# Performance work log

Measured on AMD Instinct MI355X. Metric: run time of the kernel, lower is better.

The kernel has to match this reference:

```python
import jax, jax.numpy as jnp
import numpy as np

NL = 8      # num layers (['self','cross']*4)
H = 8       # heads
EPS = 1e-5  # torch LayerNorm default


def _layernorm(x, g, b):
    mu = jnp.mean(x, axis=-1, keepdims=True)
    var = jnp.mean((x - mu) ** 2, axis=-1, keepdims=True)
    return (x - mu) * jax.lax.rsqrt(var + EPS) * g + b


def _encoder_layer(x, source, Wq, Wk, Wv, Wm, W1, W2, g1, b1, g2, b2):
    # x: [N, L, C], source: [N, S, C]
    N, L, C = x.shape
    D = C // H
    q = (x @ Wq).reshape(N, L, H, D)
    k = (source @ Wk).reshape(N, -1, H, D)
    v = (source @ Wv).reshape(N, -1, H, D)
    # naive full attention: explicit [N, L, S, H] scores (as in FullAttention)
    qk = jnp.einsum('nlhd,nshd->nlsh', q, k)
    A = jax.nn.softmax(qk * (1.0 / np.sqrt(D)), axis=2)
    msg = jnp.einsum('nlsh,nshd->nlhd', A, v).reshape(N, L, C)
    msg = _layernorm(msg @ Wm, g1, b1)
    m = jnp.concatenate([x, msg], axis=-1)          # [N, L, 2C]
    m = jax.nn.relu(m @ W1) @ W2                    # [N, L, C]
    m = _layernorm(m, g2, b2)
    return x + m


def _loftr(feat0, feat1, Wq, Wk, Wv, Wm, W1, W2, g1, b1, g2, b2):
    names = ['self', 'cross'] * 4
    for i, name in enumerate(names):
        p = (Wq[i], Wk[i], Wv[i], Wm[i], W1[i], W2[i], g1[i], b1[i], g2[i], b2[i])
        if name == 'self':
            feat0 = _encoder_layer(feat0, feat0, *p)
            feat1 = _encoder_layer(feat1, feat1, *p)
        else:  # cross; note feat0 is updated before being fed to feat1's layer
            feat0 = _encoder_layer(feat0, feat1, *p)
            feat1 = _encoder_layer(feat1, feat0, *p)
    return jnp.stack([feat0, feat1], axis=0)  # [2, N, L, C]


def setup_inputs() -> dict:
    key = jax.random.key(0)
    ks = jax.random.split(key, 10)
    N, L, C = 8, 1024, 768
    s = 1.0 / np.sqrt(C)       # xavier-ish scale for [C, C]
    s2 = 1.0 / np.sqrt(2 * C)  # for MLP fan-in 2C
    return {
        'feat0': jax.random.normal(ks[0], (N, L, C), jnp.float32),
        'feat1': jax.random.normal(ks[1], (N, L, C), jnp.float32),
        'Wq': jax.random.normal(ks[2], (NL, C, C), jnp.float32) * s,
        'Wk': jax.random.normal(ks[3], (NL, C, C), jnp.float32) * s,
        'Wv': jax.random.normal(ks[4], (NL, C, C), jnp.float32) * s,
        'Wm': jax.random.normal(ks[5], (NL, C, C), jnp.float32) * s,
        'W1': jax.random.normal(ks[6], (NL, 2 * C, 2 * C), jnp.float32) * s2,
        'W2': jax.random.normal(ks[7], (NL, 2 * C, C), jnp.float32) * s2,
        'g1': jnp.ones((NL, C), jnp.float32),
        'b1': jnp.zeros((NL, C), jnp.float32),
        'g2': jnp.ones((NL, C), jnp.float32),
        'b2': jnp.zeros((NL, C), jnp.float32),
    }


def reference(feat0, feat1, Wq, Wk, Wv, Wm, W1, W2, g1, b1, g2, b2):
    return _loftr(feat0, feat1, Wq, Wk, Wv, Wm, W1, W2, g1, b1, g2, b2)
```

## Files before the change

### kernel.cpp

```cpp
#include <hip/hip_runtime.h>
#include <hip/hip_bf16.h>

typedef __hip_bfloat16 bf16;
typedef __bf16 bf16x8 __attribute__((ext_vector_type(8)));
typedef float f32x4 __attribute__((ext_vector_type(4)));

#define AS1 __attribute__((address_space(1)))
#define AS3 __attribute__((address_space(3)))
__device__ __forceinline__ void gl_lds16(const void* g, void* l) {
    __builtin_amdgcn_global_load_lds((const AS1 void*)g, (AS3 void*)l, 16, 0, 0);
}

__device__ __forceinline__ float fexp2(float x) {
#if __has_builtin(__builtin_amdgcn_exp2f)
    return __builtin_amdgcn_exp2f(x);
#else
    return exp2f(x);
#endif
}

__device__ __forceinline__ float bf16_lo(unsigned w) { return __uint_as_float(w << 16); }
__device__ __forceinline__ float bf16_hi(unsigned w) { return __uint_as_float(w & 0xffff0000u); }

__device__ __forceinline__ int xcd_swz(int did, int nwg) {
    return (did & 7) * (nwg >> 3) + (did >> 3);
}


__global__ __launch_bounds__(256) void cvt_f32_bf16_k(const float* __restrict__ in, bf16* __restrict__ out,
                                                      int ostride, int total, float* __restrict__ xout)
{
    int i = blockIdx.x * 256 + threadIdx.x;
    int e = i * 4;
    if (e >= total) return;
    int row = e / 768;
    int col = e - row * 768;
    const float4 f = *(const float4*)(in + e);
    bf16 o4[4];
    o4[0] = __float2bfloat16(f.x); o4[1] = __float2bfloat16(f.y);
    o4[2] = __float2bfloat16(f.z); o4[3] = __float2bfloat16(f.w);
    *(uint2*)(out + (size_t)row * ostride + col) = *(uint2*)o4;
    if (xout) *(float4*)(xout + e) = f;
}

__global__ void transpose_cvt_k(const float* __restrict__ in, bf16* __restrict__ out, int R, int C,
                                float scale, size_t lstride)
{
    __shared__ float t[32][33];
    const int tx = threadIdx.x, ty = threadIdx.y;
    in  += (size_t)blockIdx.z * R * C;
    out += (size_t)blockIdx.z * lstride;
    const int c0 = blockIdx.x * 32, r0 = blockIdx.y * 32;
    #pragma unroll
    for (int i = 0; i < 4; ++i)
        t[ty + i*8][tx] = in[(size_t)(r0 + ty + i*8) * C + c0 + tx];
    __syncthreads();
    #pragma unroll
    for (int i = 0; i < 4; ++i)
        out[(size_t)(c0 + ty + i*8) * R + r0 + tx] = __float2bfloat16(t[tx][ty + i*8] * scale);
}

template<int EPI>
__global__ __launch_bounds__(256) void gemm_bt_k(const bf16* __restrict__ A, int lda,
                                                 const bf16* __restrict__ BT, int K,
                                                 void* __restrict__ Cp, int ldc,
                                                 bf16* __restrict__ Ck, bf16* __restrict__ Cv,
                                                 const bf16* __restrict__ A2)
{
    __shared__ bf16 a_sm[3][4096];
    __shared__ bf16 b_sm[3][4096];
    const int tid = threadIdx.x;
    const int lane = tid & 63;
    const int wid = tid >> 6;
    const int wr = wid >> 1, wc = wid & 1;

    const int nwg = gridDim.x * gridDim.y;
    const int did = blockIdx.x + gridDim.x * blockIdx.y;
    const int wgid = xcd_swz(did, nwg);
    const int col0 = (wgid % gridDim.y) * 128;
    const int row0 = (wgid / gridDim.y) * 128;
    const int g = lane >> 4, r16 = lane & 15;

    if (EPI == 4 && col0 >= 768) A = A2;

    const int r4 = lane >> 2;
    const int sc = (lane & 3) ^ ((lane >> 3) & 3);
    const bf16* gA[2]; const bf16* gB[2]; int loff[2];
    #pragma unroll
    for (int i = 0; i < 2; ++i) {
        const int blk = wid*2 + i;
        gA[i] = A  + (size_t)(row0 + blk*16 + r4) * lda + sc*8;
        gB[i] = BT + (size_t)(col0 + blk*16 + r4) * K   + sc*8;
        loff[i] = blk * 512;
    }
    const int foff = r16*32 + ((g ^ ((r16 >> 1) & 3)) * 8);

    f32x4 acc[4][4];
    #pragma unroll
    for (int m = 0; m < 4; ++m)
        #pragma unroll
        for (int n = 0; n < 4; ++n)
            #pragma unroll
            for (int r = 0; r < 4; ++r) acc[m][n][r] = 0.f;

    #pragma unroll
    for (int i = 0; i < 2; ++i) {
        gl_lds16(gA[i],      &a_sm[0][loff[i]]);
        gl_lds16(gB[i],      &b_sm[0][loff[i]]);
    }
    #pragma unroll
    for (int i = 0; i < 2; ++i) {
        gl_lds16(gA[i] + 32, &a_sm[1][loff[i]]);
        gl_lds16(gB[i] + 32, &b_sm[1][loff[i]]);
    }

    int cur = 0, pre = 2;
    for (int k0 = 0; k0 < K; k0 += 32) {
        if (k0 + 32 < K) asm volatile("s_waitcnt vmcnt(4)" ::: "memory");
        else             asm volatile("s_waitcnt vmcnt(0)" ::: "memory");
        __builtin_amdgcn_s_barrier();
        if (k0 + 64 < K) {
            #pragma unroll
            for (int i = 0; i < 2; ++i) {
                gl_lds16(gA[i] + k0 + 64, &a_sm[pre][loff[i]]);
                gl_lds16(gB[i] + k0 + 64, &b_sm[pre][loff[i]]);
            }
        }
        bf16x8 af[4], bfr[4];
        #pragma unroll
        for (int m = 0; m < 4; ++m) af[m]  = *(const bf16x8*)&a_sm[cur][(wr*4 + m)*512 + foff];
        #pragma unroll
        for (int n = 0; n < 4; ++n) bfr[n] = *(const bf16x8*)&b_sm[cur][(wc*4 + n)*512 + foff];
        asm volatile("s_waitcnt lgkmcnt(0)" ::: "memory");
        __builtin_amdgcn_s_setprio(1);
        #pragma unroll
        for (int m = 0; m < 4; ++m)
            #pragma unroll
            for (int n = 0; n < 4; ++n)
                acc[m][n] = __builtin_amdgcn_mfma_f32_16x16x32_bf16(af[m], bfr[n], acc[m][n], 0, 0, 0);
        __builtin_amdgcn_s_setprio(0);
        cur = (cur == 2) ? 0 : cur + 1;
        pre = (pre == 2) ? 0 : pre + 1;
    }

    #pragma unroll
    for (int m = 0; m < 4; ++m) {
        const int orow = row0 + wr*64 + m*16 + g*4;
        #pragma unroll
        for (int n = 0; n < 4; ++n) {
            const int ocol = col0 + wc*64 + n*16 + r16;
            if (EPI == 4) {
                const int seg = ocol / 768;
                const int ci = ocol - seg*768;
                if (seg <= 1) {
                    bf16* dst = (seg == 0) ? (bf16*)Cp : Ck;
                    #pragma unroll
                    for (int r = 0; r < 4; ++r)
                        dst[(size_t)(orow + r)*768 + ci] = __float2bfloat16(acc[m][n][r]);
                } else {
                    const int nn = orow >> 10, ss = orow & 1023;
                    const int hh = ci / 96, dd = ci - hh * 96;
                    bf16 pk[4];
                    #pragma unroll
                    for (int r = 0; r < 4; ++r) pk[r] = __float2bfloat16(acc[m][n][r]);
                    *(uint2*)&Cv[(((size_t)nn*8 + hh)*96 + dd)*1024 + ss] = *(uint2*)pk;
                }
            } else {
                #pragma unroll
                for (int r = 0; r < 4; ++r) {
                    float v = acc[m][n][r];
                    if (EPI == 1) v = fmaxf(v, 0.f);
                    ((bf16*)Cp)[(size_t)(orow + r)*ldc + ocol] = __float2bfloat16(v);
                }
            }
        }
    }
}

__global__ __launch_bounds__(512) void attn_k(const bf16* __restrict__ qb, const bf16* __restrict__ kb,
                                              const bf16* __restrict__ vtb, bf16* __restrict__ msgb)
{
    __shared__ bf16 kv_sm[3][12*512];
    __shared__ bf16 p_sm_all[8][32][40];
    const int tid = threadIdx.x;
    const int lane = tid & 63;
    const int w = tid >> 6;
    const int g = lane >> 4, r16 = lane & 15;

    const int nwg = gridDim.x * gridDim.y;
    const int did = blockIdx.x + gridDim.x * blockIdx.y;
    const int wgid = xcd_swz(did, nwg);
    const int qx = wgid % gridDim.x;
    const int nh = wgid / gridDim.x;
    const int n = nh >> 3, h = nh & 7;
    const int q0 = qx * 256 + w * 32;

    bf16 (*p_sm)[40] = p_sm_all[w];

    const bf16* kbase = kb  + ((size_t)n*1024)*768 + (size_t)h*96;
    const bf16* vbase = vtb + ((size_t)(n*8 + h))*96*1024;

    bf16x8 aq[2][3];
    #pragma unroll
    for (int qh = 0; qh < 2; ++qh) {
        const size_t qoff = ((size_t)n*1024 + q0 + qh*16 + r16) * 768 + (size_t)h*96;
        #pragma unroll
        for (int c = 0; c < 3; ++c) aq[qh][c] = *(const bf16x8*)&qb[qoff + c*32 + g*8];
    }

    const int r4 = lane >> 2;
    const int sc = (lane & 3) ^ ((lane >> 3) & 3);
    const bf16* gsrc[2]; size_t gstep[2]; int dstoff[2];
    const int nissue = (w < 4) ? 2 : 1;
    #pragma unroll
    for (int jj = 0; jj < 2; ++jj) {
        const int issue = w + jj*8;
        if (issue < 6) {
            const int c = issue >> 1, kh = issue & 1;
            gsrc[jj]  = kbase + (size_t)(kh*16 + r4)*768 + c*32 + sc*8;
            gstep[jj] = 768;
        } else {
            gsrc[jj]  = vbase + (size_t)((issue-6)*16 + r4)*1024 + sc*8;
            gstep[jj] = 1;
        }
        dstoff[jj] = (issue < 12) ? issue * 512 : 0;
    }
    const int foff = r16*32 + ((g ^ ((r16 >> 1) & 3)) * 8);

    float m_run[2], l_run[2];
    #pragma unroll
    for (int qh = 0; qh < 2; ++qh) { m_run[qh] = -1e30f; l_run[qh] = 0.f; }
    f32x4 o[2][6];
    #pragma unroll
    for (int qg = 0; qg < 2; ++qg)
        #pragma unroll
        for (int f = 0; f < 6; ++f)
            #pragma unroll
            for (int r = 0; r < 4; ++r) o[qg][f][r] = 0.f;

    gl_lds16(gsrc[0], &kv_sm[0][dstoff[0]]);
    if (nissue == 2) gl_lds16(gsrc[1], &kv_sm[0][dstoff[1]]);
    gl_lds16(gsrc[0] + 32 * gstep[0], &kv_sm[1][dstoff[0]]);
    if (nissue == 2) gl_lds16(gsrc[1] + 32 * gstep[1], &kv_sm[1][dstoff[1]]);

    int cur = 0, pre = 2;
    for (int kt = 0; kt < 1024; kt += 32) {
        if (kt + 32 < 1024) {
            if (nissue == 2) asm volatile("s_waitcnt vmcnt(2)" ::: "memory");
            else             asm volatile("s_waitcnt vmcnt(1)" ::: "memory");
        } else {
            asm volatile("s_waitcnt vmcnt(0)" ::: "memory");
        }
        __builtin_amdgcn_s_barrier();
        if (kt + 64 < 1024) {
            gl_lds16(gsrc[0] + (size_t)(kt + 64) * gstep[0], &kv_sm[pre][dstoff[0]]);
            if (nissue == 2) gl_lds16(gsrc[1] + (size_t)(kt + 64) * gstep[1], &kv_sm[pre][dstoff[1]]);
        }
        const bf16* rd = kv_sm[cur];

        f32x4 s[2][2];
        #pragma unroll
        for (int kh = 0; kh < 2; ++kh)
            #pragma unroll
            for (int qh = 0; qh < 2; ++qh)
                #pragma unroll
                for (int r = 0; r < 4; ++r) s[kh][qh][r] = 0.f;
        __builtin_amdgcn_s_setprio(1);
        #pragma unroll
        for (int c = 0; c < 3; ++c) {
            bf16x8 ak0 = *(const bf16x8*)&rd[(c*2 + 0)*512 + foff];
            bf16x8 ak1 = *(const bf16x8*)&rd[(c*2 + 1)*512 + foff];
            s[0][0] = __builtin_amdgcn_mfma_f32_16x16x32_bf16(ak0, aq[0][c], s[0][0], 0, 0, 0);
            s[0][1] = __builtin_amdgcn_mfma_f32_16x16x32_bf16(ak0, aq[1][c], s[0][1], 0, 0, 0);
            s[1][0] = __builtin_amdgcn_mfma_f32_16x16x32_bf16(ak1, aq[0][c], s[1][0], 0, 0, 0);
            s[1][1] = __builtin_amdgcn_mfma_f32_16x16x32_bf16(ak1, aq[1][c], s[1][1], 0, 0, 0);
        }
        __builtin_amdgcn_s_setprio(0);

        float pmv[2], gr[2];
        #pragma unroll
        for (int qh = 0; qh < 2; ++qh) {
            float pm = fmaxf(fmaxf(fmaxf(s[0][qh][0], s[0][qh][1]), fmaxf(s[0][qh][2], s[0][qh][3])),
                             fmaxf(fmaxf(s[1][qh][0], s[1][qh][1]), fmaxf(s[1][qh][2], s[1][qh][3])));
            pm = fmaxf(pm, __shfl_xor(pm, 16, 64));
            pm = fmaxf(pm, __shfl_xor(pm, 32, 64));
            pmv[qh] = pm;
            gr[qh] = pm - m_run[qh];
        }
        if (__any(fmaxf(gr[0], gr[1]) > 8.0f)) {
            float alpha_c[2];
            #pragma unroll
            for (int qh = 0; qh < 2; ++qh) {
                float mn = fmaxf(m_run[qh], pmv[qh]);
                alpha_c[qh] = fexp2(m_run[qh] - mn);
                m_run[qh] = mn;
                l_run[qh] *= alpha_c[qh];
            }
            #pragma unroll
            for (int qg = 0; qg < 2; ++qg)
                #pragma unroll
                for (int r = 0; r < 4; ++r) {
                    float ar = __shfl(alpha_c[qg], g*4 + r, 64);
                    #pragma unroll
                    for (int f = 0; f < 6; ++f) o[qg][f][r] *= ar;
                }
        }
        #pragma unroll
        for (int qh = 0; qh < 2; ++qh) {
            bf16 pk0[4], pk1[4];
            float rs = 0.f;
            #pragma unroll
            for (int r = 0; r < 4; ++r) {
                float p0 = fexp2(s[0][qh][r] - m_run[qh]);
                float p1 = fexp2(s[1][qh][r] - m_run[qh]);
                rs += p0 + p1;
                pk0[r] = __float2bfloat16(p0);
                pk1[r] = __float2bfloat16(p1);
            }
            rs += __shfl_xor(rs, 16, 64);
            rs += __shfl_xor(rs, 32, 64);
            l_run[qh] += rs;
            *(uint2*)&p_sm[qh*16 + r16][g*4]      = *(uint2*)pk0;
            *(uint2*)&p_sm[qh*16 + r16][16 + g*4] = *(uint2*)pk1;
        }

        bf16x8 pa0 = *(const bf16x8*)&p_sm[r16][g*8];
        bf16x8 pa1 = *(const bf16x8*)&p_sm[16 + r16][g*8];
        __builtin_amdgcn_s_setprio(1);
        #pragma unroll
        for (int f = 0; f < 6; ++f) {
            bf16x8 bv = *(const bf16x8*)&rd[(6 + f)*512 + foff];
            o[0][f] = __builtin_amdgcn_mfma_f32_16x16x32_bf16(pa0, bv, o[0][f], 0, 0, 0);
            o[1][f] = __builtin_amdgcn_mfma_f32_16x16x32_bf16(pa1, bv, o[1][f], 0, 0, 0);
        }
        __builtin_amdgcn_s_setprio(0);
        asm volatile("s_waitcnt lgkmcnt(0)" ::: "memory");
        cur = (cur == 2) ? 0 : cur + 1;
        pre = (pre == 2) ? 0 : pre + 1;
    }

    float linv[2][4];
    #pragma unroll
    for (int qg = 0; qg < 2; ++qg)
        #pragma unroll
        for (int r = 0; r < 4; ++r)
            linv[qg][r] = 1.0f / __shfl(l_run[qg], g*4 + r, 64);

    #pragma unroll
    for (int qg = 0; qg < 2; ++qg) {
        const size_t obase = ((size_t)n*1024 + q0 + qg*16 + g*4) * 768 + (size_t)h*96;
        #pragma unroll
        for (int f = 0; f < 6; ++f)
            #pragma unroll
            for (int r = 0; r < 4; ++r)
                msgb[obase + (size_t)r*768 + f*16 + r16] = __float2bfloat16(o[qg][f][r] * linv[qg][r]);
    }
}

template<int MODE>
__global__ __launch_bounds__(256) void ln_k(const bf16* __restrict__ in, const float* __restrict__ g,
                                            const float* __restrict__ b, bf16* __restrict__ outc,
                                            float* __restrict__ x)
{
    const int lane = threadIdx.x & 63;
    const int w = threadIdx.x >> 6;
    const int row = blockIdx.x * 4 + w;
    const bf16* rp = in + (size_t)row * 768;
    const int c1 = lane * 8, c2 = 512 + lane * 4;

    const uint4 u1 = *(const uint4*)&rp[c1];
    const uint2 u2 = *(const uint2*)&rp[c2];
    float f1[8], f2[4];
    f1[0] = bf16_lo(u1.x); f1[1] = bf16_hi(u1.x);
    f1[2] = bf16_lo(u1.y); f1[3] = bf16_hi(u1.y);
    f1[4] = bf16_lo(u1.z); f1[5] = bf16_hi(u1.z);
    f1[6] = bf16_lo(u1.w); f1[7] = bf16_hi(u1.w);
    f2[0] = bf16_lo(u2.x); f2[1] = bf16_hi(u2.x);
    f2[2] = bf16_lo(u2.y); f2[3] = bf16_hi(u2.y);
    float s = 0.f, sq = 0.f;
    #pragma unroll
    for (int j = 0; j < 8; ++j) { s += f1[j]; sq += f1[j]*f1[j]; }
    #pragma unroll
    for (int j = 0; j < 4; ++j) { s += f2[j]; sq += f2[j]*f2[j]; }
    #pragma unroll
    for (int off = 1; off < 64; off <<= 1) {
        s  += __shfl_xor(s,  off, 64);
        sq += __shfl_xor(sq, off, 64);
    }
    const float mu = s * (1.f/768.f);
    float var = sq * (1.f/768.f) - mu*mu;
    var = fmaxf(var, 0.f);
    const float rs = rsqrtf(var + 1e-5f);

    const float4 ga  = *(const float4*)&g[c1];
    const float4 gb4 = *(const float4*)&g[c1 + 4];
    const float4 gc  = *(const float4*)&g[c2];
    const float4 ba  = *(const float4*)&b[c1];
    const float4 bb4 = *(const float4*)&b[c1 + 4];
    const float4 bc  = *(const float4*)&b[c2];
    float y1[8], y2[4];
    y1[0] = (f1[0]-mu)*rs*ga.x + ba.x;   y1[1] = (f1[1]-mu)*rs*ga.y + ba.y;
    y1[2] = (f1[2]-mu)*rs*ga.z + ba.z;   y1[3] = (f1[3]-mu)*rs*ga.w + ba.w;
    y1[4] = (f1[4]-mu)*rs*gb4.x + bb4.x; y1[5] = (f1[5]-mu)*rs*gb4.y + bb4.y;
    y1[6] = (f1[6]-mu)*rs*gb4.z + bb4.z; y1[7] = (f1[7]-mu)*rs*gb4.w + bb4.w;
    y2[0] = (f2[0]-mu)*rs*gc.x + bc.x;   y2[1] = (f2[1]-mu)*rs*gc.y + bc.y;
    y2[2] = (f2[2]-mu)*rs*gc.z + bc.z;   y2[3] = (f2[3]-mu)*rs*gc.w + bc.w;

    if (MODE == 1) {
        bf16 o1[8], o2[4];
        #pragma unroll
        for (int j = 0; j < 8; ++j) o1[j] = __float2bfloat16(y1[j]);
        #pragma unroll
        for (int j = 0; j < 4; ++j) o2[j] = __float2bfloat16(y2[j]);
        *(uint4*)&outc[(size_t)row*1536 + 768 + c1] = *(uint4*)o1;
        *(uint2*)&outc[(size_t)row*1536 + 768 + c2] = *(uint2*)o2;
    } else {
        float* xr = x + (size_t)row * 768;
        float4 xa = *(float4*)&xr[c1];
        float4 xb = *(float4*)&xr[c1 + 4];
        float4 xc = *(float4*)&xr[c2];
        xa.x += y1[0]; xa.y += y1[1]; xa.z += y1[2]; xa.w += y1[3];
        xb.x += y1[4]; xb.y += y1[5]; xb.z += y1[6]; xb.w += y1[7];
        xc.x += y2[0]; xc.y += y2[1]; xc.z += y2[2]; xc.w += y2[3];
        *(float4*)&xr[c1]     = xa;
        *(float4*)&xr[c1 + 4] = xb;
        *(float4*)&xr[c2]     = xc;
        bf16 o1[8], o2[4];
        o1[0] = __float2bfloat16(xa.x); o1[1] = __float2bfloat16(xa.y);
        o1[2] = __float2bfloat16(xa.z); o1[3] = __float2bfloat16(xa.w);
        o1[4] = __float2bfloat16(xb.x); o1[5] = __float2bfloat16(xb.y);
        o1[6] = __float2bfloat16(xb.z); o1[7] = __float2bfloat16(xb.w);
        o2[0] = __float2bfloat16(xc.x); o2[1] = __float2bfloat16(xc.y);
        o2[2] = __float2bfloat16(xc.z); o2[3] = __float2bfloat16(xc.w);
        *(uint4*)&outc[(size_t)row*1536 + c1] = *(uint4*)o1;
        *(uint2*)&outc[(size_t)row*1536 + c2] = *(uint2*)o2;
    }
}

extern "C" void kernel_launch(void* const* d_in, const int* in_sizes, int n_in,
                              void* d_out, int out_size, void* d_ws, size_t ws_size,
                              hipStream_t stream)
{
    const float* feat0 = (const float*)d_in[0];
    const float* feat1 = (const float*)d_in[1];
    const float* Wq = (const float*)d_in[2];
    const float* Wk = (const float*)d_in[3];
    const float* Wv = (const float*)d_in[4];
    const float* Wm = (const float*)d_in[5];
    const float* W1 = (const float*)d_in[6];
    const float* W2 = (const float*)d_in[7];
    const float* g1 = (const float*)d_in[8];
    const float* b1 = (const float*)d_in[9];
    const float* g2 = (const float*)d_in[10];
    const float* b2 = (const float*)d_in[11];

    bf16 *wqkvT, *wmT, *w1T, *w2T, *concat0, *concat1, *qb, *kb, *vtb, *m1b, *t0b;
    auto plan = [&](int RB) -> size_t {
        char* p = (char*)d_ws;
        auto take = [&](size_t bytes) { char* q = p; p += (bytes + 255) & ~(size_t)255; return q; };
        wqkvT = (bf16*)take((size_t)8*2304*768*2);
        wmT  = (bf16*)take((size_t)8*768*768*2);
        w1T  = (bf16*)take((size_t)8*1536*1536*2);
        w2T  = (bf16*)take((size_t)8*768*1536*2);
        concat0 = (bf16*)take((size_t)8192*1536*2);
        concat1 = (bf16*)take((size_t)8192*1536*2);
        qb   = (bf16*)take((size_t)RB*768*2);
        kb   = (bf16*)take((size_t)RB*768*2);
        vtb  = (bf16*)take((size_t)RB*768*2);
        m1b  = (bf16*)take((size_t)RB*1536*2);
        t0b  = (bf16*)take((size_t)RB*768*2);
        return (size_t)(p - (char*)d_ws);
    };
    bool batched = plan(16384) <= ws_size;
    if (!batched) plan(8192);
    bf16* msgb = qb;

    float* x0 = (float*)d_out;
    float* x1 = x0 + (size_t)8192*768;

    const float s_qk = 0.14724444f;
    const dim3 tb(32, 8);
    const size_t QKV = (size_t)2304*768;
    transpose_cvt_k<<<dim3(24,24,8), tb, 0, stream>>>(Wq, wqkvT,            768, 768,  s_qk, QKV);
    transpose_cvt_k<<<dim3(24,24,8), tb, 0, stream>>>(Wk, wqkvT + 768*768,  768, 768,  1.0f, QKV);
    transpose_cvt_k<<<dim3(24,24,8), tb, 0, stream>>>(Wv, wqkvT + 1536*768, 768, 768,  1.0f, QKV);
    transpose_cvt_k<<<dim3(24,24,8), tb, 0, stream>>>(Wm, wmT, 768, 768,  1.0f, (size_t)768*768);
    transpose_cvt_k<<<dim3(48,48,8), tb, 0, stream>>>(W1, w1T, 1536, 1536, 1.0f, (size_t)1536*1536);
    transpose_cvt_k<<<dim3(24,48,8), tb, 0, stream>>>(W2, w2T, 1536, 768,  1.0f, (size_t)1536*768);

    const int total = 8192*768;
    cvt_f32_bf16_k<<<6144, 256, 0, stream>>>(feat0, concat0, 1536, total, x0);
    cvt_f32_bf16_k<<<6144, 256, 0, stream>>>(feat1, concat1, 1536, total, x1);

    auto encode = [&](float* x, bf16* cS, const bf16* cR, int i, int M) {
        const bf16* wl = wqkvT + (size_t)i * QKV;
        const int MT = M / 128;
        gemm_bt_k<4><<<dim3(MT,18), 256, 0, stream>>>(cS, 1536, wl, 768, qb, 768, kb, vtb, cR);
        attn_k<<<dim3(4, (M/1024)*8), 512, 0, stream>>>(qb, kb, vtb, msgb);
        gemm_bt_k<0><<<dim3(MT,6),  256, 0, stream>>>(msgb, 768, wmT + (size_t)i*768*768, 768,
                                                      t0b, 768, nullptr, nullptr, nullptr);
        ln_k<1><<<M/4, 256, 0, stream>>>(t0b, g1 + i*768, b1 + i*768, cS, nullptr);
        gemm_bt_k<1><<<dim3(MT,12), 256, 0, stream>>>(cS, 1536, w1T + (size_t)i*1536*1536, 1536,
                                                      m1b, 1536, nullptr, nullptr, nullptr);
        gemm_bt_k<0><<<dim3(MT,6),  256, 0, stream>>>(m1b, 1536, w2T + (size_t)i*768*1536, 1536,
                                                      t0b, 768, nullptr, nullptr, nullptr);
        ln_k<2><<<M/4, 256, 0, stream>>>(t0b, g2 + i*768, b2 + i*768, cS, x);
    };

    for (int i = 0; i < 8; ++i) {
        if ((i & 1) == 0) {
            if (batched) {
                encode(x0, concat0, concat0, i, 16384);
            } else {
                encode(x0, concat0, concat0, i, 8192);
                encode(x1, concat1, concat1, i, 8192);
            }
        } else {
            encode(x0, concat0, concat1, i, 8192);
            encode(x1, concat1, concat0, i, 8192);
        }
    }
}
```

Baseline: 3.352 ms.

## Add 256x256-tile 8-wave GEMM kernel for QKV and MLP projections

```diff
diff --git a/kernel.cpp b/kernel.cpp
--- a/kernel.cpp
+++ b/kernel.cpp
@@ -81,8 +81,6 @@
     const int row0 = (wgid / gridDim.y) * 128;
     const int g = lane >> 4, r16 = lane & 15;
 
-    if (EPI == 4 && col0 >= 768) A = A2;
-
     const int r4 = lane >> 2;
     const int sc = (lane & 3) ^ ((lane >> 3) & 3);
     const bf16* gA[2]; const bf16* gB[2]; int loff[2];
@@ -146,6 +144,140 @@
     #pragma unroll
     for (int m = 0; m < 4; ++m) {
         const int orow = row0 + wr*64 + m*16 + g*4;
+        #pragma unroll
+        for (int n = 0; n < 4; ++n) {
+            const int ocol = col0 + wc*64 + n*16 + r16;
+            #pragma unroll
+            for (int r = 0; r < 4; ++r) {
+                float v = acc[m][n][r];
+                if (EPI == 1) v = fmaxf(v, 0.f);
+                ((bf16*)Cp)[(size_t)(orow + r)*ldc + ocol] = __float2bfloat16(v);
+            }
+        }
+    }
+}
+
+template<int EPI>
+__global__ __launch_bounds__(512) void gemm8_k(const bf16* __restrict__ A, int lda,
+                                               const bf16* __restrict__ BT, int K,
+                                               void* __restrict__ Cp, int ldc,
+                                               bf16* __restrict__ Ck, bf16* __restrict__ Cv,
+                                               const bf16* __restrict__ A2)
+{
+    __shared__ bf16 a_sm[2][16384];
+    __shared__ bf16 b_sm[2][16384];
+    const int tid = threadIdx.x;
+    const int lane = tid & 63;
+    const int wid = tid >> 6;
+    const int wr = wid >> 2, wc = wid & 3;
+
+    const int nwg = gridDim.x * gridDim.y;
+    const int did = blockIdx.x + gridDim.x * blockIdx.y;
+    const int wgid = xcd_swz(did, nwg);
+    const int col0 = (wgid % gridDim.y) * 256;
+    const int row0 = (wgid / gridDim.y) * 256;
+    const int g = lane >> 4, r16 = lane & 15;
+
+    if (EPI == 4 && col0 >= 768) A = A2;
+
+    const int r4 = lane >> 2;
+    const int sc = (lane & 3) ^ ((lane >> 3) & 3);
+    const bf16* gA0 = A  + (size_t)(row0 + (wid*2+0)*16 + r4) * lda + sc*8;
+    const bf16* gA1 = A  + (size_t)(row0 + (wid*2+1)*16 + r4) * lda + sc*8;
+    const bf16* gB0 = BT + (size_t)(col0 + (wid*2+0)*16 + r4) * K   + sc*8;
+    const bf16* gB1 = BT + (size_t)(col0 + (wid*2+1)*16 + r4) * K   + sc*8;
+    const int l0 = (wid*2+0)*1024;
+    const int l1 = (wid*2+1)*1024;
+
+    const int foff = r16*32 + ((g ^ ((r16 >> 1) & 3)) * 8);
+
+    f32x4 acc[8][4];
+    #pragma unroll
+    for (int m = 0; m < 8; ++m)
+        #pragma unroll
+        for (int n = 0; n < 4; ++n)
+            #pragma unroll
+            for (int r = 0; r < 4; ++r) acc[m][n][r] = 0.f;
+
+    gl_lds16(gA0,      &a_sm[0][l0]);
+    gl_lds16(gA1,      &a_sm[0][l1]);
+    gl_lds16(gB0,      &b_sm[0][l0]);
+    gl_lds16(gB1,      &b_sm[0][l1]);
+    gl_lds16(gA0 + 32, &a_sm[0][l0 + 512]);
+    gl_lds16(gA1 + 32, &a_sm[0][l1 + 512]);
+    gl_lds16(gB0 + 32, &b_sm[0][l0 + 512]);
+    gl_lds16(gB1 + 32, &b_sm[0][l1 + 512]);
+    asm volatile("s_waitcnt vmcnt(0)" ::: "memory");
+    __builtin_amdgcn_s_barrier();
+
+#define QMFMA(BASE) do {                                                                     \
+    __builtin_amdgcn_s_setprio(1);                                                           \
+    _Pragma("unroll")                                                                        \
+    for (int m = 0; m < 4; ++m)                                                              \
+        _Pragma("unroll")                                                                    \
+        for (int n = 0; n < 4; ++n)                                                          \
+            acc[(BASE)+m][n] = __builtin_amdgcn_mfma_f32_16x16x32_bf16(af[m], bfv[n], acc[(BASE)+m][n], 0, 0, 0); \
+    __builtin_amdgcn_s_setprio(0);                                                           \
+} while (0)
+
+    const int NT = K >> 6;
+    int buf = 0;
+    for (int t = 0; t < NT; ++t) {
+        const int nb = buf ^ 1;
+        const int kn = (t + 1) << 6;
+        const bool hn = (t + 1) < NT;
+        bf16x8 af[4], bfv[4];
+
+        #pragma unroll
+        for (int m = 0; m < 4; ++m) af[m]  = *(const bf16x8*)&a_sm[buf][((wr*8 + m)*2 + 0)*512 + foff];
+        #pragma unroll
+        for (int n = 0; n < 4; ++n) bfv[n] = *(const bf16x8*)&b_sm[buf][((wc*4 + n)*2 + 0)*512 + foff];
+        if (hn) { gl_lds16(gA0 + kn, &a_sm[nb][l0]); gl_lds16(gA1 + kn, &a_sm[nb][l1]); }
+        __builtin_amdgcn_s_barrier();
+        asm volatile("s_waitcnt lgkmcnt(0)" ::: "memory");
+        __builtin_amdgcn_sched_barrier(0);
+        QMFMA(0);
+        __builtin_amdgcn_s_barrier();
+
+        #pragma unroll
+        for (int m = 0; m < 4; ++m) af[m] = *(const bf16x8*)&a_sm[buf][((wr*8 + 4 + m)*2 + 0)*512 + foff];
+        if (hn) { gl_lds16(gB0 + kn, &b_sm[nb][l0]); gl_lds16(gB1 + kn, &b_sm[nb][l1]); }
+        __builtin_amdgcn_s_barrier();
+        asm volatile("s_waitcnt lgkmcnt(0)" ::: "memory");
+        __builtin_amdgcn_sched_barrier(0);
+        QMFMA(4);
+        if (hn) asm volatile("s_waitcnt vmcnt(4)" ::: "memory");
+        else    asm volatile("s_waitcnt vmcnt(0)" ::: "memory");
+        __builtin_amdgcn_s_barrier();
+
+        #pragma unroll
+        for (int m = 0; m < 4; ++m) af[m]  = *(const bf16x8*)&a_sm[buf][((wr*8 + m)*2 + 1)*512 + foff];
+        #pragma unroll
+        for (int n = 0; n < 4; ++n) bfv[n] = *(const bf16x8*)&b_sm[buf][((wc*4 + n)*2 + 1)*512 + foff];
+        if (hn) { gl_lds16(gA0 + kn + 32, &a_sm[nb][l0 + 512]); gl_lds16(gA1 + kn + 32, &a_sm[nb][l1 + 512]); }
+        __builtin_amdgcn_s_barrier();
+        asm volatile("s_waitcnt lgkmcnt(0)" ::: "memory");
+        __builtin_amdgcn_sched_barrier(0);
+        QMFMA(0);
+        __builtin_amdgcn_s_barrier();
+
+        #pragma unroll
+        for (int m = 0; m < 4; ++m) af[m] = *(const bf16x8*)&a_sm[buf][((wr*8 + 4 + m)*2 + 1)*512 + foff];
+        if (hn) { gl_lds16(gB0 + kn + 32, &b_sm[nb][l0 + 512]); gl_lds16(gB1 + kn + 32, &b_sm[nb][l1 + 512]); }
+        __builtin_amdgcn_s_barrier();
+        asm volatile("s_waitcnt lgkmcnt(0)" ::: "memory");
+        __builtin_amdgcn_sched_barrier(0);
+        QMFMA(4);
+        if (hn) asm volatile("s_waitcnt vmcnt(4)" ::: "memory");
+        __builtin_amdgcn_s_barrier();
+
+        buf = nb;
+    }
+#undef QMFMA
+
+    #pragma unroll
+    for (int m = 0; m < 8; ++m) {
+        const int orow = row0 + wr*128 + m*16 + g*4;
         #pragma unroll
         for (int n = 0; n < 4; ++n) {
             const int ocol = col0 + wc*64 + n*16 + r16;
@@ -494,16 +626,24 @@
 
     auto encode = [&](float* x, bf16* cS, const bf16* cR, int i, int M) {
         const bf16* wl = wqkvT + (size_t)i * QKV;
-        const int MT = M / 128;
-        gemm_bt_k<4><<<dim3(MT,18), 256, 0, stream>>>(cS, 1536, wl, 768, qb, 768, kb, vtb, cR);
+        const int MT8 = M / 256;
+        gemm8_k<4><<<dim3(MT8, 9), 512, 0, stream>>>(cS, 1536, wl, 768, qb, 768, kb, vtb, cR);
         attn_k<<<dim3(4, (M/1024)*8), 512, 0, stream>>>(qb, kb, vtb, msgb);
-        gemm_bt_k<0><<<dim3(MT,6),  256, 0, stream>>>(msgb, 768, wmT + (size_t)i*768*768, 768,
-                                                      t0b, 768, nullptr, nullptr, nullptr);
+        if (M == 16384)
+            gemm8_k<0><<<dim3(MT8, 3), 512, 0, stream>>>(msgb, 768, wmT + (size_t)i*768*768, 768,
+                                                         t0b, 768, nullptr, nullptr, nullptr);
+        else
+            gemm_bt_k<0><<<dim3(M/128, 6), 256, 0, stream>>>(msgb, 768, wmT + (size_t)i*768*768, 768,
+                                                             t0b, 768, nullptr, nullptr, nullptr);
         ln_k<1><<<M/4, 256, 0, stream>>>(t0b, g1 + i*768, b1 + i*768, cS, nullptr);
-        gemm_bt_k<1><<<dim3(MT,12), 256, 0, stream>>>(cS, 1536, w1T + (size_t)i*1536*1536, 1536,
-                                                      m1b, 1536, nullptr, nullptr, nullptr);
-        gemm_bt_k<0><<<dim3(MT,6),  256, 0, stream>>>(m1b, 1536, w2T + (size_t)i*768*1536, 1536,
-                                                      t0b, 768, nullptr, nullptr, nullptr);
+        gemm8_k<1><<<dim3(MT8, 6), 512, 0, stream>>>(cS, 1536, w1T + (size_t)i*1536*1536, 1536,
+                                                     m1b, 1536, nullptr, nullptr, nullptr);
+        if (M == 16384)
+            gemm8_k<0><<<dim3(MT8, 3), 512, 0, stream>>>(m1b, 1536, w2T + (size_t)i*768*1536, 1536,
+                                                         t0b, 768, nullptr, nullptr, nullptr);
+        else
+            gemm_bt_k<0><<<dim3(M/128, 6), 256, 0, stream>>>(m1b, 1536, w2T + (size_t)i*768*1536, 1536,
+                                                             t0b, 768, nullptr, nullptr, nullptr);
         ln_k<2><<<M/4, 256, 0, stream>>>(t0b, g2 + i*768, b2 + i*768, cS, x);
     };
 
```

Measured after the change: 3.509 ms. +4.7%, slower.
